# Kernel tuning notes

Hardware: AMD Instinct MI355X
Metric: run time of the kernel (lower is better)

Reference implementation:

```python
import jax, jax.numpy as jnp
import numpy as np

B, H, S, D = 2, 8, 4096, 64
EPS = 1e-12  # torch F.normalize default eps

def _l2_normalize(x):
    n = jnp.linalg.norm(x, axis=-1, keepdims=True)
    return x / jnp.maximum(n, EPS)

def setup_inputs() -> dict:
    key = jax.random.key(0)
    kq, kk, kv, km = jax.random.split(key, 4)
    return {
        "query": jax.random.normal(kq, (B, H, S, D), dtype=jnp.float32),
        "key": jax.random.normal(kk, (B, H, S, D), dtype=jnp.float32),
        "value": jax.random.normal(kv, (B, H, S, D), dtype=jnp.float32),
        "mask": jax.random.randint(km, (B, 1, 1, S), 0, 2, dtype=jnp.int32),
    }

def reference(query, key, value, mask):
    q = _l2_normalize(query)
    k = _l2_normalize(key)
    # [B,H,S,S] cosine-similarity scores
    scores = jnp.einsum("bhqd,bhkd->bhqk", q, k)
    scores = jnp.where(mask == 0, jnp.float32(-1.0), scores)
    scores = (scores + 1.0) * 0.5  # map [-1,1] -> [0,1]; masked entries -> 0
    attention = scores / jnp.sum(scores, axis=-1, keepdims=True)
    return jnp.einsum("bhqk,bhkd->bhqd", attention, value)
```

## Files before the change

kernel.cpp:

```cpp
#include <hip/hip_runtime.h>


#define S 4096
#define D 64
#define BH 16
#define FSTRIDE 4352
#define NE 4225
#define NCHM 32
#define NCHO 64
#define KSTR 40
#define QSTR 72

typedef __attribute__((ext_vector_type(8))) short short8;
typedef __attribute__((ext_vector_type(4))) float f32x4;

__device__ __forceinline__ float rl(float v, int l) {
    return __int_as_float(__builtin_amdgcn_readlane(__float_as_int(v), l));
}
__device__ __forceinline__ unsigned bf16h(float x) {
    unsigned u = __float_as_uint(x);
    u += 0x7FFF + ((u >> 16) & 1);
    return u >> 16;
}

__global__ __launch_bounds__(256) void k_moments(
    const float* __restrict__ K, const float* __restrict__ V,
    const int* __restrict__ mask, float* __restrict__ part)
{
    __shared__ float red[4 * 4096];
    __shared__ float sured[4 * 132];
    unsigned short* stag = (unsigned short*)red;

    const int bh    = blockIdx.x;
    const int chunk = blockIdx.y;
    const int tid   = threadIdx.x;
    const int lane  = tid & 63;
    const int wave  = tid >> 6;
    const int quad  = lane >> 4;
    const int l15   = lane & 15;
    const int row0  = chunk * 128 + wave * 32;

    const float* Kh = K + (size_t)bh * S * D;
    const float* Vh = V + (size_t)bh * S * D;
    const int*   mb = mask + (bh >> 3) * S;

    const int r32 = lane & 31;
    const int c2  = lane >> 5;
    const int rowA = row0 + r32;
    float ss = 0.f;
    {
        const float4* kp = (const float4*)(Kh + (size_t)rowA * D + c2 * 32);
        #pragma unroll
        for (int i = 0; i < 8; ++i) {
            float4 kv = kp[i];
            ss = fmaf(kv.x, kv.x, ss);
            ss = fmaf(kv.y, kv.y, ss);
            ss = fmaf(kv.z, kv.z, ss);
            ss = fmaf(kv.w, kv.w, ss);
        }
    }
    ss += __shfl_xor(ss, 32, 64);
    const float mval = (float)mb[rowA];
    const float minv = mval / fmaxf(sqrtf(ss), 1e-12f);

    unsigned short* KstT = stag + wave * (64 * KSTR);
    unsigned short* VstT = stag + 4 * (64 * KSTR) + wave * (64 * KSTR);
    unsigned* KstW = (unsigned*)KstT;
    unsigned* VstW = (unsigned*)VstT;

    float s_acc = 0.f, u_acc = 0.f, n_acc = 0.f;
    unsigned kprev = 0, vprev = 0;
    #pragma unroll
    for (int r = 0; r < 32; ++r) {
        const int row = row0 + r;
        float kd = Kh[(size_t)row * D + lane];
        float vd = Vh[(size_t)row * D + lane];
        float aj = rl(minv, r);
        float mj = rl(mval, r);
        float kh = kd * aj;
        float vm = vd * mj;
        s_acc += kh; u_acc += vm; n_acc += mj;
        unsigned ku = bf16h(kh), vu = bf16h(vm);
        if (r & 1) {
            KstW[(lane * KSTR + (r - 1)) >> 1] = kprev | (ku << 16);
            VstW[(lane * KSTR + (r - 1)) >> 1] = vprev | (vu << 16);
        } else { kprev = ku; vprev = vu; }
    }
    __syncthreads();

    short8 af[4], bfr[4];
    #pragma unroll
    for (int t = 0; t < 4; ++t) {
        af[t]  = *(const short8*)(KstT + (t * 16 + l15) * KSTR + quad * 8);
        bfr[t] = *(const short8*)(VstT + (t * 16 + l15) * KSTR + quad * 8);
    }
    f32x4 acc[4][4];
    #pragma unroll
    for (int tm = 0; tm < 4; ++tm)
        #pragma unroll
        for (int tn = 0; tn < 4; ++tn)
            acc[tm][tn] = (f32x4){0.f, 0.f, 0.f, 0.f};
    #pragma unroll
    for (int tn = 0; tn < 4; ++tn)
        #pragma unroll
        for (int tm = 0; tm < 4; ++tm)
            acc[tm][tn] = __builtin_amdgcn_mfma_f32_16x16x32_bf16(
                af[tm], bfr[tn], acc[tm][tn], 0, 0, 0);
    __syncthreads();

    #pragma unroll
    for (int tm = 0; tm < 4; ++tm)
        #pragma unroll
        for (int tn = 0; tn < 4; ++tn)
            #pragma unroll
            for (int rr = 0; rr < 4; ++rr)
                red[wave * 4096 + (tm * 16 + quad * 4 + rr) * 64 + tn * 16 + l15]
                    = acc[tm][tn][rr];
    sured[wave * 132 + lane]      = s_acc;
    sured[wave * 132 + 64 + lane] = u_acc;
    if (lane == 0) sured[wave * 132 + 128] = n_acc;
    __syncthreads();

    float* pp = part + ((size_t)bh * NCHM + chunk) * FSTRIDE;
    for (int i = tid; i < NE; i += 256) {
        float v;
        if (i < 4096)
            v = red[i] + red[4096 + i] + red[8192 + i] + red[12288 + i];
        else {
            int e = i - 4096;
            v = sured[e] + sured[132 + e] + sured[264 + e] + sured[396 + e];
        }
        pp[i] = v;
    }
}

__global__ __launch_bounds__(256) void k_reduce(
    const float* __restrict__ part, float* __restrict__ fin,
    unsigned short* __restrict__ finTh)
{
    const int bh = blockIdx.x;
    const int e  = blockIdx.y * 256 + threadIdx.x;
    if (e >= NE) return;
    const float* p = part + (size_t)bh * NCHM * FSTRIDE + e;
    float a0 = 0.f, a1 = 0.f, a2 = 0.f, a3 = 0.f;
    #pragma unroll
    for (int c = 0; c < NCHM; c += 4) {
        a0 += p[(size_t)(c + 0) * FSTRIDE];
        a1 += p[(size_t)(c + 1) * FSTRIDE];
        a2 += p[(size_t)(c + 2) * FSTRIDE];
        a3 += p[(size_t)(c + 3) * FSTRIDE];
    }
    float v = (a0 + a1) + (a2 + a3);
    if (e < 4096)
        finTh[(size_t)bh * 4096 + (e & 63) * 64 + (e >> 6)] = (unsigned short)bf16h(v);
    else
        fin[(size_t)bh * FSTRIDE + e] = v;
}

__global__ __launch_bounds__(256) void k_out(
    const float* __restrict__ Q, const float* __restrict__ fin,
    const unsigned short* __restrict__ finTh, float* __restrict__ out)
{
    __shared__ unsigned short Qst[4 * 16 * QSTR];

    const int bh    = blockIdx.x;
    const int chunk = blockIdx.y;
    const int tid   = threadIdx.x;
    const int lane  = tid & 63;
    const int wave  = tid >> 6;
    const int quad  = lane >> 4;
    const int l15   = lane & 15;
    const int row0  = chunk * 64;

    const float* fb = fin + (size_t)bh * FSTRIDE;
    const unsigned short* fT = finTh + (size_t)bh * 4096;
    const float* Qh = Q + (size_t)bh * S * D;
    float*       Oh = out + (size_t)bh * S * D;

    const int rowA = row0 + wave * 16 + l15;
    float ss = 0.f, qs = 0.f;
    {
        const float4* qp = (const float4*)(Qh + (size_t)rowA * D + quad * 16);
        const float4* sp = (const float4*)(fb + 4096 + quad * 16);
        #pragma unroll
        for (int i = 0; i < 4; ++i) {
            float4 qv = qp[i], sv = sp[i];
            ss = fmaf(qv.x, qv.x, ss);
            ss = fmaf(qv.y, qv.y, ss);
            ss = fmaf(qv.z, qv.z, ss);
            ss = fmaf(qv.w, qv.w, ss);
            qs = fmaf(qv.x, sv.x, qs);
            qs = fmaf(qv.y, sv.y, qs);
            qs = fmaf(qv.z, sv.z, qs);
            qs = fmaf(qv.w, sv.w, qs);
        }
    }
    ss += __shfl_xor(ss, 16, 64); ss += __shfl_xor(ss, 32, 64);
    qs += __shfl_xor(qs, 16, 64); qs += __shfl_xor(qs, 32, 64);
    const float nval = fb[4224];
    const float invL = 1.f / fmaxf(sqrtf(ss), 1e-12f);
    const float rden = 1.f / fmaf(qs, invL, nval);

    unsigned short* Qw = Qst + wave * 16 * QSTR;
    #pragma unroll
    for (int r = 0; r < 16; ++r) {
        float qd = Qh[(size_t)(row0 + wave * 16 + r) * D + lane];
        Qw[r * QSTR + lane] = (unsigned short)bf16h(qd * rl(invL, r));
    }
    asm volatile("" ::: "memory");

    short8 af0 = *(const short8*)(Qw + l15 * QSTR + quad * 8);
    short8 af1 = *(const short8*)(Qw + l15 * QSTR + 32 + quad * 8);

    f32x4 acc[4];
    #pragma unroll
    for (int tn = 0; tn < 4; ++tn) acc[tn] = (f32x4){0.f, 0.f, 0.f, 0.f};
    #pragma unroll
    for (int tn = 0; tn < 4; ++tn) {
        short8 b0 = *(const short8*)(fT + (tn * 16 + l15) * 64 + quad * 8);
        short8 b1 = *(const short8*)(fT + (tn * 16 + l15) * 64 + 32 + quad * 8);
        acc[tn] = __builtin_amdgcn_mfma_f32_16x16x32_bf16(af0, b0, acc[tn], 0, 0, 0);
        acc[tn] = __builtin_amdgcn_mfma_f32_16x16x32_bf16(af1, b1, acc[tn], 0, 0, 0);
    }

    float u4[4];
    #pragma unroll
    for (int tn = 0; tn < 4; ++tn) u4[tn] = fb[4160 + tn * 16 + l15];

    #pragma unroll
    for (int rr = 0; rr < 4; ++rr) {
        const int src = quad * 4 + rr;
        float rd = __int_as_float(
            __builtin_amdgcn_ds_bpermute(src << 2, __float_as_int(rden)));
        const size_t row = row0 + wave * 16 + src;
        #pragma unroll
        for (int tn = 0; tn < 4; ++tn)
            Oh[row * D + tn * 16 + l15] = (acc[tn][rr] + u4[tn]) * rd;
    }
}

extern "C" void kernel_launch(void* const* d_in, const int* in_sizes, int n_in,
                              void* d_out, int out_size, void* d_ws, size_t ws_size,
                              hipStream_t stream) {
    const float* Q    = (const float*)d_in[0];
    const float* K    = (const float*)d_in[1];
    const float* V    = (const float*)d_in[2];
    const int*   mask = (const int*)d_in[3];
    float* out = (float*)d_out;
    float* ws  = (float*)d_ws;

    float*          fin   = ws;
    unsigned short* finTh = (unsigned short*)(ws + (size_t)BH * FSTRIDE);
    float*          part  = (float*)((char*)finTh + (size_t)BH * 4096 * 2);

    k_moments<<<dim3(BH, NCHM), 256, 0, stream>>>(K, V, mask, part);
    k_reduce <<<dim3(BH, (NE + 255) / 256), 256, 0, stream>>>(part, fin, finTh);
    k_out    <<<dim3(BH, NCHO), 256, 0, stream>>>(Q, fin, finTh, out);
}
```

Before: 107.9 us.

## Shrink moments-kernel LDS footprint and vectorize K/V staging loads

```diff
diff --git a/kernel.cpp b/kernel.cpp
--- a/kernel.cpp
+++ b/kernel.cpp
@@ -8,14 +8,19 @@
 #define NE 4225
 #define NCHM 32
 #define NCHO 64
-#define KSTR 40
+#define KSTR 36
 #define QSTR 72
 
 typedef __attribute__((ext_vector_type(8))) short short8;
+typedef __attribute__((ext_vector_type(4))) short short4v;
 typedef __attribute__((ext_vector_type(4))) float f32x4;
 
 __device__ __forceinline__ float rl(float v, int l) {
     return __int_as_float(__builtin_amdgcn_readlane(__float_as_int(v), l));
+}
+__device__ __forceinline__ float bperm(float v, int srclane) {
+    return __int_as_float(
+        __builtin_amdgcn_ds_bpermute(srclane << 2, __float_as_int(v)));
 }
 __device__ __forceinline__ unsigned bf16h(float x) {
     unsigned u = __float_as_uint(x);
@@ -23,13 +28,14 @@
     return u >> 16;
 }
 
-__global__ __launch_bounds__(256) void k_moments(
+__global__ __launch_bounds__(256, 4) void k_moments(
     const float* __restrict__ K, const float* __restrict__ V,
     const int* __restrict__ mask, float* __restrict__ part)
 {
-    __shared__ float red[4 * 4096];
+    __shared__ unsigned short stag[8 * 64 * KSTR];
     __shared__ float sured[4 * 132];
-    unsigned short* stag = (unsigned short*)red;
+    float* red0 = (float*)stag;
+    float* red1 = red0 + 4096;
 
     const int bh    = blockIdx.x;
     const int chunk = blockIdx.y;
@@ -62,37 +68,79 @@
     ss += __shfl_xor(ss, 32, 64);
     const float mval = (float)mb[rowA];
     const float minv = mval / fmaxf(sqrtf(ss), 1e-12f);
-
-    unsigned short* KstT = stag + wave * (64 * KSTR);
-    unsigned short* VstT = stag + 4 * (64 * KSTR) + wave * (64 * KSTR);
-    unsigned* KstW = (unsigned*)KstT;
-    unsigned* VstW = (unsigned*)VstT;
-
-    float s_acc = 0.f, u_acc = 0.f, n_acc = 0.f;
-    unsigned kprev = 0, vprev = 0;
-    #pragma unroll
-    for (int r = 0; r < 32; ++r) {
-        const int row = row0 + r;
-        float kd = Kh[(size_t)row * D + lane];
-        float vd = Vh[(size_t)row * D + lane];
-        float aj = rl(minv, r);
-        float mj = rl(mval, r);
-        float kh = kd * aj;
-        float vm = vd * mj;
-        s_acc += kh; u_acc += vm; n_acc += mj;
-        unsigned ku = bf16h(kh), vu = bf16h(vm);
-        if (r & 1) {
-            KstW[(lane * KSTR + (r - 1)) >> 1] = kprev | (ku << 16);
-            VstW[(lane * KSTR + (r - 1)) >> 1] = vprev | (vu << 16);
-        } else { kprev = ku; vprev = vu; }
-    }
+    float nw = mval;
+    nw += __shfl_xor(nw, 1, 64);  nw += __shfl_xor(nw, 2, 64);
+    nw += __shfl_xor(nw, 4, 64);  nw += __shfl_xor(nw, 8, 64);
+    nw += __shfl_xor(nw, 16, 64); nw += __shfl_xor(nw, 32, 64);
+
+    unsigned short* Kst = stag + wave * (64 * KSTR);
+    unsigned short* Vst = stag + 4 * (64 * KSTR) + wave * (64 * KSTR);
+    unsigned* KstW = (unsigned*)Kst;
+    unsigned* VstW = (unsigned*)Vst;
+
+    float4 s4 = {0.f, 0.f, 0.f, 0.f}, u4 = {0.f, 0.f, 0.f, 0.f};
+    unsigned kprev[4], vprev[4];
+    #pragma unroll
+    for (int i = 0; i < 8; ++i) {
+        const int key = 8 * quad + i;
+        const int row = row0 + key;
+        float4 kf = *(const float4*)(Kh + (size_t)row * D + 4 * l15);
+        float4 vf = *(const float4*)(Vh + (size_t)row * D + 4 * l15);
+        float aj = bperm(minv, key);
+        float mj = bperm(mval, key);
+        float k0 = kf.x * aj, k1 = kf.y * aj, k2 = kf.z * aj, k3 = kf.w * aj;
+        float v0 = vf.x * mj, v1 = vf.y * mj, v2 = vf.z * mj, v3 = vf.w * mj;
+        s4.x += k0; s4.y += k1; s4.z += k2; s4.w += k3;
+        u4.x += v0; u4.y += v1; u4.z += v2; u4.w += v3;
+        unsigned kb0 = bf16h(k0), kb1 = bf16h(k1), kb2 = bf16h(k2), kb3 = bf16h(k3);
+        unsigned vb0 = bf16h(v0), vb1 = bf16h(v1), vb2 = bf16h(v2), vb3 = bf16h(v3);
+        if (i & 1) {
+            const int base = 4 * quad + (i >> 1);
+            KstW[(4 * l15 + 0) * 18 + base] = kprev[0] | (kb0 << 16);
+            KstW[(4 * l15 + 1) * 18 + base] = kprev[1] | (kb1 << 16);
+            KstW[(4 * l15 + 2) * 18 + base] = kprev[2] | (kb2 << 16);
+            KstW[(4 * l15 + 3) * 18 + base] = kprev[3] | (kb3 << 16);
+            VstW[(4 * l15 + 0) * 18 + base] = vprev[0] | (vb0 << 16);
+            VstW[(4 * l15 + 1) * 18 + base] = vprev[1] | (vb1 << 16);
+            VstW[(4 * l15 + 2) * 18 + base] = vprev[2] | (vb2 << 16);
+            VstW[(4 * l15 + 3) * 18 + base] = vprev[3] | (vb3 << 16);
+        } else {
+            kprev[0] = kb0; kprev[1] = kb1; kprev[2] = kb2; kprev[3] = kb3;
+            vprev[0] = vb0; vprev[1] = vb1; vprev[2] = vb2; vprev[3] = vb3;
+        }
+    }
+    s4.x += __shfl_xor(s4.x, 16, 64); s4.x += __shfl_xor(s4.x, 32, 64);
+    s4.y += __shfl_xor(s4.y, 16, 64); s4.y += __shfl_xor(s4.y, 32, 64);
+    s4.z += __shfl_xor(s4.z, 16, 64); s4.z += __shfl_xor(s4.z, 32, 64);
+    s4.w += __shfl_xor(s4.w, 16, 64); s4.w += __shfl_xor(s4.w, 32, 64);
+    u4.x += __shfl_xor(u4.x, 16, 64); u4.x += __shfl_xor(u4.x, 32, 64);
+    u4.y += __shfl_xor(u4.y, 16, 64); u4.y += __shfl_xor(u4.y, 32, 64);
+    u4.z += __shfl_xor(u4.z, 16, 64); u4.z += __shfl_xor(u4.z, 32, 64);
+    u4.w += __shfl_xor(u4.w, 16, 64); u4.w += __shfl_xor(u4.w, 32, 64);
+    if (quad == 0) {
+        sured[wave * 132 + 4 * l15 + 0]      = s4.x;
+        sured[wave * 132 + 4 * l15 + 1]      = s4.y;
+        sured[wave * 132 + 4 * l15 + 2]      = s4.z;
+        sured[wave * 132 + 4 * l15 + 3]      = s4.w;
+        sured[wave * 132 + 64 + 4 * l15 + 0] = u4.x;
+        sured[wave * 132 + 64 + 4 * l15 + 1] = u4.y;
+        sured[wave * 132 + 64 + 4 * l15 + 2] = u4.z;
+        sured[wave * 132 + 64 + 4 * l15 + 3] = u4.w;
+    }
+    if (lane == 0) sured[wave * 132 + 128] = nw * 0.5f;
     __syncthreads();
 
     short8 af[4], bfr[4];
     #pragma unroll
     for (int t = 0; t < 4; ++t) {
-        af[t]  = *(const short8*)(KstT + (t * 16 + l15) * KSTR + quad * 8);
-        bfr[t] = *(const short8*)(VstT + (t * 16 + l15) * KSTR + quad * 8);
+        const unsigned short* ab = Kst + (t * 16 + l15) * KSTR + quad * 8;
+        short4v a0 = *(const short4v*)ab;
+        short4v a1 = *(const short4v*)(ab + 4);
+        af[t] = __builtin_shufflevector(a0, a1, 0, 1, 2, 3, 4, 5, 6, 7);
+        const unsigned short* bb = Vst + (t * 16 + l15) * KSTR + quad * 8;
+        short4v b0 = *(const short4v*)bb;
+        short4v b1 = *(const short4v*)(bb + 4);
+        bfr[t] = __builtin_shufflevector(b0, b1, 0, 1, 2, 3, 4, 5, 6, 7);
     }
     f32x4 acc[4][4];
     #pragma unroll
@@ -108,24 +156,36 @@
                 af[tm], bfr[tn], acc[tm][tn], 0, 0, 0);
     __syncthreads();
 
-    #pragma unroll
-    for (int tm = 0; tm < 4; ++tm)
-        #pragma unroll
-        for (int tn = 0; tn < 4; ++tn)
+    if (wave < 2) {
+        float* rd = wave ? red1 : red0;
+        #pragma unroll
+        for (int tm = 0; tm < 4; ++tm)
             #pragma unroll
-            for (int rr = 0; rr < 4; ++rr)
-                red[wave * 4096 + (tm * 16 + quad * 4 + rr) * 64 + tn * 16 + l15]
-                    = acc[tm][tn][rr];
-    sured[wave * 132 + lane]      = s_acc;
-    sured[wave * 132 + 64 + lane] = u_acc;
-    if (lane == 0) sured[wave * 132 + 128] = n_acc;
+            for (int tn = 0; tn < 4; ++tn)
+                #pragma unroll
+                for (int rr = 0; rr < 4; ++rr)
+                    rd[(tm * 16 + quad * 4 + rr) * 64 + tn * 16 + l15]
+                        = acc[tm][tn][rr];
+    }
+    __syncthreads();
+    if (wave >= 2) {
+        float* rd = (wave == 3) ? red1 : red0;
+        #pragma unroll
+        for (int tm = 0; tm < 4; ++tm)
+            #pragma unroll
+            for (int tn = 0; tn < 4; ++tn)
+                #pragma unroll
+                for (int rr = 0; rr < 4; ++rr)
+                    rd[(tm * 16 + quad * 4 + rr) * 64 + tn * 16 + l15]
+                        += acc[tm][tn][rr];
+    }
     __syncthreads();
 
     float* pp = part + ((size_t)bh * NCHM + chunk) * FSTRIDE;
     for (int i = tid; i < NE; i += 256) {
         float v;
         if (i < 4096)
-            v = red[i] + red[4096 + i] + red[8192 + i] + red[12288 + i];
+            v = red0[i] + red1[i];
         else {
             int e = i - 4096;
             v = sured[e] + sured[132 + e] + sured[264 + e] + sured[396 + e];
@@ -230,8 +290,7 @@
     #pragma unroll
     for (int rr = 0; rr < 4; ++rr) {
         const int src = quad * 4 + rr;
-        float rd = __int_as_float(
-            __builtin_amdgcn_ds_bpermute(src << 2, __float_as_int(rden)));
+        float rd = bperm(rden, src);
         const size_t row = row0 + wave * 16 + src;
         #pragma unroll
         for (int tn = 0; tn < 4; ++tn)
```

Measured after the change: 107.8 us. No clear change (-0.1%).
